# Performance work log

Measured on AMD Instinct MI355X. Metric: run time of the kernel, lower is better.

Reference implementation:

```python
import jax, jax.numpy as jnp
import numpy as np

NUM_ATOMS = 50000
NUM_EDGES = 200000  # even: edges come in (fwd, rev) pairs
D_V, D_E, D_H = 133, 14, 256
DEPTH = 3


def setup_inputs() -> dict:
    key = jax.random.key(0)
    ks = jax.random.split(key, 12)
    half = NUM_EDGES // 2
    src = jax.random.randint(ks[0], (half,), 0, NUM_ATOMS)
    dst = jax.random.randint(ks[1], (half,), 0, NUM_ATOMS)
    v = jnp.concatenate([src, dst])
    w = jnp.concatenate([dst, src])
    edge_index = jnp.stack([v, w])  # [2, E]
    rev_edge_index = jnp.concatenate([jnp.arange(half) + half, jnp.arange(half)])

    def lin(k, out_d, in_d):
        return jax.random.normal(k, (out_d, in_d), jnp.float32) / np.sqrt(in_d)

    return {
        "V": jax.random.normal(ks[2], (NUM_ATOMS, D_V), jnp.float32),
        "E_feat": jax.random.normal(ks[3], (NUM_EDGES, D_E), jnp.float32),
        "edge_index": edge_index,
        "rev_edge_index": rev_edge_index,
        "Wi_atom": lin(ks[4], D_H, D_V),
        "Wi_bond": lin(ks[5], D_H, D_V + D_E),
        "Wh_atom": lin(ks[6], D_H, D_H),
        "Wh_bond": lin(ks[7], D_H, D_H),
        "Wf_atom": lin(ks[8], D_H, D_H),
        "Wf_bond": lin(ks[9], D_H, D_H),
        "Wo_atom": lin(ks[10], D_H, D_V + D_H),
    }


def _sum_and_max_into_atoms(H_e, w_idx, num_atoms):
    a_sum = jax.ops.segment_sum(H_e, w_idx, num_segments=num_atoms)
    a_max = jax.ops.segment_max(H_e, w_idx, num_segments=num_atoms)
    a_max = jnp.where(jnp.isfinite(a_max), a_max, 0.0)  # empty segments -> 0
    return a_sum, a_max


def _fuse(H, m, Wf):
    # Fusion(kind='mlp', residual=True), dropout=0:
    # residual update with a small MLP on the combined signal
    return H + jax.nn.relu((H + m) @ Wf.T)


def reference(V, E_feat, edge_index, rev_edge_index, Wi_atom, Wi_bond,
              Wh_atom, Wh_bond, Wf_atom, Wf_bond, Wo_atom):
    tau = jax.nn.relu
    num_atoms = V.shape[0]
    v = edge_index[0]
    w = edge_index[1]

    H_a = tau(V @ Wi_atom.T)                                        # [N, d_h]
    H_b = tau(jnp.concatenate([V[v], E_feat], axis=1) @ Wi_bond.T)  # [E, d_h]

    for _ in range(1, DEPTH):
        a_sum, a_max = _sum_and_max_into_atoms(H_b, w, num_atoms)
        gate = a_sum * a_max
        m_a = gate @ Wh_atom.T
        H_a = _fuse(H_a, m_a, Wf_atom)

        M_b = a_sum[v] - H_b[rev_edge_index]
        m_b = M_b @ Wh_bond.T
        H_b = _fuse(H_b, m_b, Wf_bond)

    a_sum, _ = _sum_and_max_into_atoms(H_b, w, num_atoms)
    H_atom = tau(jnp.concatenate([V, a_sum], axis=1) @ Wo_atom.T)   # [N, d_h]
    return H_atom
```

## Files before the change

kernel.cpp:

```cpp
#include <hip/hip_runtime.h>
#include <hip/hip_bf16.h>

#define NATOM 50000
#define NEDGE 200000
#define HALF  100000
#define DV    133
#define DE    14
#define DH    256
#define KVP   160
#define NBLK_SCAN ((NATOM + 255) / 256)

typedef __bf16  bf16x8 __attribute__((ext_vector_type(8)));
typedef __bf16  bf16x4 __attribute__((ext_vector_type(4)));
typedef float   f32x4  __attribute__((ext_vector_type(4)));

__device__ __forceinline__ void gll16(const void* g, void* l) {
    __builtin_amdgcn_global_load_lds(
        (const __attribute__((address_space(1))) unsigned int*)g,
        (__attribute__((address_space(3))) unsigned int*)l, 16, 0, 0);
}
__device__ __forceinline__ void drain_barrier() {
    __builtin_amdgcn_s_waitcnt(0);
    __syncthreads();
}
__device__ __forceinline__ int swz(int row, int byteInRow) {
    return row * 512 + (byteInRow ^ ((row & 7) << 4));
}


struct DArgs {
    const float* Vf; const float* Ef; const float* asumf;
    const int* vidx;
    const __bf16* W1; const __bf16* W2;
    __bf16* C; float* Cf;
    int M;
};

template<int MODE, int KITERS>
__global__ __launch_bounds__(512, 4) void dgemm(DArgs g) {
    const int tid = threadIdx.x;
    const int lane = tid & 63, wv = tid >> 6;
    const int quad = lane >> 4, l16 = lane & 15;
    const int wr = (wv >> 2) * 64, wc = (wv & 3) * 64;
    const int gr0 = blockIdx.x * 128;

    int vrow[4]; const float* epp[4];
#pragma unroll
    for (int m = 0; m < 4; ++m) {
        int r = gr0 + wr + m * 16 + l16;
        if (r > g.M - 1) r = g.M - 1;
        vrow[m] = (MODE == 1) ? g.vidx[r] : r;
        epp[m] = (MODE == 1) ? (g.Ef + (size_t)r * DE) : nullptr;
    }

    f32x4 acc[16];
#pragma unroll
    for (int i = 0; i < 16; ++i) acc[i] = (f32x4){0.f, 0.f, 0.f, 0.f};

#pragma unroll
    for (int kk = 0; kk < KITERS; ++kk) {
        bf16x8 af[4];
#pragma unroll
        for (int m = 0; m < 4; ++m) {
            const int cb = kk * 32 + quad * 8;
            if (MODE != 2 || kk < 5) {
                const float* vp = g.Vf + (size_t)vrow[m] * DV;
                if (kk < 4) {
                    f32x4 x0, x1;
                    __builtin_memcpy(&x0, vp + cb, 16);
                    __builtin_memcpy(&x1, vp + cb + 4, 16);
#pragma unroll
                    for (int j = 0; j < 4; ++j) {
                        af[m][j] = (__bf16)x0[j]; af[m][4 + j] = (__bf16)x1[j];
                    }
                } else {
#pragma unroll
                    for (int j = 0; j < 8; ++j) {
                        int c = cb + j; float y = 0.f;
                        if (c < DV) y = vp[c];
                        else if (MODE == 1 && c < DV + DE) y = epp[m][c - DV];
                        af[m][j] = (__bf16)y;
                    }
                }
            } else {
                const float* sp = g.asumf + (size_t)vrow[m] * DH + (kk - 5) * 32 + quad * 8;
                f32x4 s0 = *(const f32x4*)sp, s1 = *(const f32x4*)(sp + 4);
#pragma unroll
                for (int j = 0; j < 4; ++j) {
                    af[m][j] = (__bf16)s0[j]; af[m][4 + j] = (__bf16)s1[j];
                }
            }
        }
        bf16x8 bfv[4];
#pragma unroll
        for (int n = 0; n < 4; ++n) {
            int col = wc + n * 16 + l16;
            const __bf16* wp;
            if (MODE == 2 && kk >= 5) wp = g.W2 + (size_t)col * DH  + (kk - 5) * 32 + quad * 8;
            else                      wp = g.W1 + (size_t)col * KVP + kk * 32 + quad * 8;
            bfv[n] = *(const bf16x8*)wp;
        }
#pragma unroll
        for (int m = 0; m < 4; ++m)
#pragma unroll
            for (int n = 0; n < 4; ++n)
                acc[m * 4 + n] = __builtin_amdgcn_mfma_f32_16x16x32_bf16(
                    af[m], bfv[n], acc[m * 4 + n], 0, 0, 0);
    }

#pragma unroll
    for (int m = 0; m < 4; ++m)
#pragma unroll
    for (int n = 0; n < 4; ++n)
#pragma unroll
    for (int r = 0; r < 4; ++r) {
        int gr = gr0 + wr + m * 16 + quad * 4 + r;
        if (gr < g.M) {
            int col = wc + n * 16 + l16;
            float v = acc[m * 4 + n][r];
            v = v > 0.f ? v : 0.f;
            if (MODE == 2) g.Cf[(size_t)gr * DH + col] = v;
            else           g.C [(size_t)gr * DH + col] = (__bf16)v;
        }
    }
}

struct FArgs {
    const float* asumf; const __bf16* asumb; const __bf16* amaxb;
    const int* vidx;
    const __bf16* W1; const __bf16* W2;
    __bf16* H;
    int M;
};

template<int BOND>
__global__ __launch_bounds__(512, 4) void fgemm(FArgs g) {
    __shared__ __bf16 Hlds[16384];
    __shared__ __bf16 Alds[16384];
    const int tid = threadIdx.x;
    const int lane = tid & 63, wv = tid >> 6;
    const int quad = lane >> 4, l16 = lane & 15;
    const int wr = (wv >> 2) * 32;
    const int wc = (wv & 3) * 64;
    const int bid = blockIdx.x;

    int garow[2];
    if (!BOND) {
#pragma unroll
        for (int fr = 0; fr < 2; ++fr) {
            int r = bid * 64 + wr + fr * 16 + l16;
            if (r > g.M - 1) r = g.M - 1;
            garow[fr] = r;
        }
    }

#pragma unroll
    for (int it = 0; it < 4; ++it) {
        int unit = it * 512 + wv * 64 + lane;
        int lr = unit >> 5, u16 = unit & 31;
        int swzoff = (u16 * 16) ^ ((lr & 7) << 4);
        int srow;
        if (BOND) { int sl = bid * 32 + (lr & 31); srow = (lr < 32) ? sl : HALF + sl; }
        else      { srow = bid * 64 + lr; if (srow > g.M - 1) srow = g.M - 1; }
        gll16((const char*)g.H + (size_t)srow * 512 + swzoff,
              (char*)Hlds + it * 8192 + wv * 1024);
        if (BOND) {
            int sl = bid * 32 + (lr & 31);
            int gA = (lr < 32) ? sl : HALF + sl;
            int grow = g.vidx[gA];
            gll16((const char*)g.asumb + (size_t)grow * 512 + swzoff,
                  (char*)Alds + it * 8192 + wv * 1024);
        }
    }
    drain_barrier();

    f32x4 acc[8];
#pragma unroll
    for (int i = 0; i < 8; ++i) acc[i] = (f32x4){0.f, 0.f, 0.f, 0.f};

#pragma unroll
    for (int kk = 0; kk < 8; ++kk) {
        const int cb = kk * 32 + quad * 8;
        bf16x8 mf[2];
#pragma unroll
        for (int fr = 0; fr < 2; ++fr) {
            int lr = wr + fr * 16 + l16;
            if (BOND) {
                bf16x8 a = *(const bf16x8*)((const char*)Alds + swz(lr, cb * 2));
                bf16x8 h = *(const bf16x8*)((const char*)Hlds + swz(lr ^ 32, cb * 2));
#pragma unroll
                for (int j = 0; j < 8; ++j)
                    mf[fr][j] = (__bf16)((float)a[j] - (float)h[j]);
            } else {
                const float* s = g.asumf + (size_t)garow[fr] * DH + cb;
                f32x4 s0 = *(const f32x4*)s, s1 = *(const f32x4*)(s + 4);
                bf16x8 mx = *(const bf16x8*)(g.amaxb + (size_t)garow[fr] * DH + cb);
#pragma unroll
                for (int j = 0; j < 4; ++j) {
                    mf[fr][j]     = (__bf16)(s0[j] * (float)mx[j]);
                    mf[fr][4 + j] = (__bf16)(s1[j] * (float)mx[4 + j]);
                }
            }
        }
        bf16x8 wf[4];
#pragma unroll
        for (int fc = 0; fc < 4; ++fc)
            wf[fc] = *(const bf16x8*)(g.W1 + (size_t)(wc + fc * 16 + l16) * DH + cb);
#pragma unroll
        for (int fc = 0; fc < 4; ++fc)
#pragma unroll
            for (int fr = 0; fr < 2; ++fr)
                acc[fc * 2 + fr] = __builtin_amdgcn_mfma_f32_16x16x32_bf16(
                    wf[fc], mf[fr], acc[fc * 2 + fr], 0, 0, 0);
    }
    drain_barrier();

#pragma unroll
    for (int fc = 0; fc < 4; ++fc)
#pragma unroll
    for (int fr = 0; fr < 2; ++fr) {
        int row = wr + fr * 16 + l16;
        int colb = wc + fc * 16 + quad * 4;
        int off = swz(row, colb * 2);
        bf16x4 h = *(const bf16x4*)((const char*)Hlds + off);
        bf16x4 t;
#pragma unroll
        for (int j = 0; j < 4; ++j)
            t[j] = (__bf16)((float)h[j] + acc[fc * 2 + fr][j]);
        *(bf16x4*)((char*)Alds + off) = t;
    }
    drain_barrier();

#pragma unroll
    for (int i = 0; i < 8; ++i) acc[i] = (f32x4){0.f, 0.f, 0.f, 0.f};
#pragma unroll
    for (int kk = 0; kk < 8; ++kk) {
        const int cb = kk * 32 + quad * 8;
        bf16x8 tf[2];
#pragma unroll
        for (int fr = 0; fr < 2; ++fr) {
            int lr = wr + fr * 16 + l16;
            tf[fr] = *(const bf16x8*)((const char*)Alds + swz(lr, cb * 2));
        }
        bf16x8 wf[4];
#pragma unroll
        for (int fc = 0; fc < 4; ++fc)
            wf[fc] = *(const bf16x8*)(g.W2 + (size_t)(wc + fc * 16 + l16) * DH + cb);
#pragma unroll
        for (int fc = 0; fc < 4; ++fc)
#pragma unroll
            for (int fr = 0; fr < 2; ++fr)
                acc[fc * 2 + fr] = __builtin_amdgcn_mfma_f32_16x16x32_bf16(
                    wf[fc], tf[fr], acc[fc * 2 + fr], 0, 0, 0);
    }

#pragma unroll
    for (int fc = 0; fc < 4; ++fc)
#pragma unroll
    for (int fr = 0; fr < 2; ++fr) {
        int row = wr + fr * 16 + l16;
        int colb = wc + fc * 16 + quad * 4;
        int off = swz(row, colb * 2);
        bf16x4 h = *(const bf16x4*)((const char*)Hlds + off);
        bf16x4 o;
#pragma unroll
        for (int j = 0; j < 4; ++j) {
            float v = acc[fc * 2 + fr][j];
            v = v > 0.f ? v : 0.f;
            o[j] = (__bf16)((float)h[j] + v);
        }
        *(bf16x4*)((char*)Hlds + off) = o;
    }
    drain_barrier();

#pragma unroll
    for (int it = 0; it < 4; ++it) {
        int unit = it * 512 + tid;
        int lr = unit >> 5, u16 = unit & 31;
        bool ok; int srow;
        if (BOND) { int sl = bid * 32 + (lr & 31); ok = true; srow = (lr < 32) ? sl : HALF + sl; }
        else      { srow = bid * 64 + lr; ok = srow < g.M; }
        if (ok) {
            bf16x8 v = *(const bf16x8*)((const char*)Hlds + swz(lr, u16 * 16));
            *(bf16x8*)((char*)g.H + (size_t)srow * 512 + u16 * 16) = v;
        }
    }
}

__global__ void count_deg(const int* __restrict__ widx, int* __restrict__ cnt) {
    int e = blockIdx.x * 256 + threadIdx.x;
    if (e < NEDGE) atomicAdd(&cnt[widx[e]], 1);
}

__global__ __launch_bounds__(256) void scan_p1(const int* __restrict__ cnt,
                                               int* __restrict__ rowptr,
                                               int* __restrict__ bsum) {
    __shared__ int sm[256];
    const int tid = threadIdx.x;
    const int i = blockIdx.x * 256 + tid;
    int v = (i < NATOM) ? cnt[i] : 0;
    sm[tid] = v;
    __syncthreads();
    for (int off = 1; off < 256; off <<= 1) {
        int t = (tid >= off) ? sm[tid - off] : 0;
        __syncthreads();
        sm[tid] += t;
        __syncthreads();
    }
    if (i < NATOM) rowptr[i] = sm[tid] - v;
    if (tid == 255) bsum[blockIdx.x] = sm[255];
}

__global__ __launch_bounds__(256) void scan_p2(int* __restrict__ bsum) {
    __shared__ int sm[256];
    const int tid = threadIdx.x;
    int v = (tid < NBLK_SCAN) ? bsum[tid] : 0;
    sm[tid] = v;
    __syncthreads();
    for (int off = 1; off < 256; off <<= 1) {
        int t = (tid >= off) ? sm[tid - off] : 0;
        __syncthreads();
        sm[tid] += t;
        __syncthreads();
    }
    if (tid < NBLK_SCAN) bsum[tid] = sm[tid] - v;
    if (tid == 255) bsum[NBLK_SCAN] = sm[255];
}

__global__ __launch_bounds__(256) void scan_p3(int* __restrict__ rowptr,
                                               int* __restrict__ cursor,
                                               const int* __restrict__ bsum) {
    const int i = blockIdx.x * 256 + threadIdx.x;
    if (i < NATOM) {
        int r = rowptr[i] + bsum[blockIdx.x];
        rowptr[i] = r;
        cursor[i] = r;
    }
    if (i == 0) rowptr[NATOM] = bsum[NBLK_SCAN];
}

__global__ void fill_csr(const int* __restrict__ widx, int* __restrict__ cursor,
                         int* __restrict__ eid) {
    int e = blockIdx.x * 256 + threadIdx.x;
    if (e >= NEDGE) return;
    int pos = atomicAdd(&cursor[widx[e]], 1);
    eid[pos] = e;
}

template<int WITHMAX>
__global__ __launch_bounds__(256) void seg_reduce(
    const __bf16* __restrict__ Hb, const int* __restrict__ rowptr,
    const int* __restrict__ eid,
    float* __restrict__ asum, __bf16* __restrict__ asumb,
    __bf16* __restrict__ amaxb)
{
    int a = blockIdx.x * 4 + (threadIdx.x >> 6);
    if (a >= NATOM) return;
    const int lane = threadIdx.x & 63;
    const int beg = rowptr[a], end = rowptr[a + 1];
    float s0 = 0.f, s1 = 0.f, s2 = 0.f, s3 = 0.f;
    float m0 = 0.f, m1 = 0.f, m2 = 0.f, m3 = 0.f;
    for (int i = beg; i < end; ++i) {
        int e = eid[i];
        bf16x4 h = *(const bf16x4*)(Hb + (size_t)e * DH + lane * 4);
        float v0 = (float)h[0], v1 = (float)h[1], v2 = (float)h[2], v3 = (float)h[3];
        s0 += v0; s1 += v1; s2 += v2; s3 += v3;
        if (WITHMAX) {
            m0 = fmaxf(m0, v0); m1 = fmaxf(m1, v1);
            m2 = fmaxf(m2, v2); m3 = fmaxf(m3, v3);
        }
    }
    size_t o = (size_t)a * DH + lane * 4;
    *(f32x4*)(asum + o) = (f32x4){s0, s1, s2, s3};
    if (WITHMAX) {
        bf16x4 sv; sv[0] = (__bf16)s0; sv[1] = (__bf16)s1; sv[2] = (__bf16)s2; sv[3] = (__bf16)s3;
        *(bf16x4*)(asumb + o) = sv;
        bf16x4 mv; mv[0] = (__bf16)m0; mv[1] = (__bf16)m1; mv[2] = (__bf16)m2; mv[3] = (__bf16)m3;
        *(bf16x4*)(amaxb + o) = mv;
    }
}

__global__ void pad_w2(const float* __restrict__ src, __bf16* __restrict__ dst,
                       int srcld, int coloff, int KS, int KD) {
    int i = blockIdx.x * 256 + threadIdx.x;
    if (i >= 256 * KD) return;
    int n = i / KD, c = i - n * KD;
    dst[i] = (c < KS) ? (__bf16)src[(size_t)n * srcld + coloff + c] : (__bf16)0.f;
}

static inline int cdiv(long a, long b) { return (int)((a + b - 1) / b); }

extern "C" void kernel_launch(void* const* d_in, const int* in_sizes, int n_in,
                              void* d_out, int out_size, void* d_ws, size_t ws_size,
                              hipStream_t stream) {
    const float* V    = (const float*)d_in[0];
    const float* Ef   = (const float*)d_in[1];
    const int*   ei   = (const int*)d_in[2];
    const int*   rev  = (const int*)d_in[3];
    const float* Wi_a = (const float*)d_in[4];
    const float* Wi_b = (const float*)d_in[5];
    const float* Wh_a = (const float*)d_in[6];
    const float* Wh_b = (const float*)d_in[7];
    const float* Wf_a = (const float*)d_in[8];
    const float* Wf_b = (const float*)d_in[9];
    const float* Wo   = (const float*)d_in[10];
    float* out = (float*)d_out;
    (void)rev;

    const int* vidx = ei;
    const int* widx = ei + NEDGE;

    char* ws = (char*)d_ws;
    __bf16* Hb    = (__bf16*)(ws + 0);
    __bf16* Ha    = (__bf16*)(ws + 102400000);
    float*  asum  = (float*) (ws + 128000000);
    __bf16* asumb = (__bf16*)(ws + 179200000);
    __bf16* amaxb = (__bf16*)(ws + 204800000);
    __bf16* Wia   = (__bf16*)(ws + 230400000);
    __bf16* Wib   = (__bf16*)(ws + 230481920);
    __bf16* Wo1   = (__bf16*)(ws + 230563840);
    __bf16* Wo2   = (__bf16*)(ws + 230645760);
    __bf16* Wha   = (__bf16*)(ws + 230776832);
    __bf16* Whb   = (__bf16*)(ws + 230907904);
    __bf16* Wfa   = (__bf16*)(ws + 231038976);
    __bf16* Wfb   = (__bf16*)(ws + 231170048);
    int*  rowptr  = (int*)(ws + 231301120);
    int*  cursor  = (int*)(ws + 231501312);
    int*  eid     = (int*)(ws + 231701504);
    int*  bsum    = (int*)(ws + 232501504);
    (void)ws_size;

    hipMemsetAsync(cursor, 0, NATOM * sizeof(int), stream);
    count_deg<<<cdiv(NEDGE, 256), 256, 0, stream>>>(widx, cursor);
    scan_p1<<<NBLK_SCAN, 256, 0, stream>>>(cursor, rowptr, bsum);
    scan_p2<<<1, 256, 0, stream>>>(bsum);
    scan_p3<<<NBLK_SCAN, 256, 0, stream>>>(rowptr, cursor, bsum);
    fill_csr<<<cdiv(NEDGE, 256), 256, 0, stream>>>(widx, cursor, eid);

    pad_w2<<<cdiv(256 * KVP, 256), 256, 0, stream>>>(Wi_a, Wia, DV, 0, DV, KVP);
    pad_w2<<<cdiv(256 * KVP, 256), 256, 0, stream>>>(Wi_b, Wib, DV + DE, 0, DV + DE, KVP);
    pad_w2<<<cdiv(256 * KVP, 256), 256, 0, stream>>>(Wo, Wo1, DV + DH, 0, DV, KVP);
    pad_w2<<<cdiv(256 * DH, 256), 256, 0, stream>>>(Wo, Wo2, DV + DH, DV, DH, DH);
    pad_w2<<<cdiv(256 * DH, 256), 256, 0, stream>>>(Wh_a, Wha, DH, 0, DH, DH);
    pad_w2<<<cdiv(256 * DH, 256), 256, 0, stream>>>(Wh_b, Whb, DH, 0, DH, DH);
    pad_w2<<<cdiv(256 * DH, 256), 256, 0, stream>>>(Wf_a, Wfa, DH, 0, DH, DH);
    pad_w2<<<cdiv(256 * DH, 256), 256, 0, stream>>>(Wf_b, Wfb, DH, 0, DH, DH);

    {
        DArgs d{}; d.Vf = V; d.W1 = Wia; d.C = Ha; d.M = NATOM;
        dgemm<0, 5><<<cdiv(NATOM, 128), 512, 0, stream>>>(d);
    }
    {
        DArgs d{}; d.Vf = V; d.Ef = Ef; d.vidx = vidx; d.W1 = Wib; d.C = Hb; d.M = NEDGE;
        dgemm<1, 5><<<cdiv(NEDGE, 128), 512, 0, stream>>>(d);
    }

    for (int it = 0; it < 2; ++it) {
        seg_reduce<1><<<cdiv(NATOM, 4), 256, 0, stream>>>(Hb, rowptr, eid, asum, asumb, amaxb);
        {
            FArgs f{}; f.asumf = asum; f.amaxb = amaxb;
            f.W1 = Wha; f.W2 = Wfa; f.H = Ha; f.M = NATOM;
            fgemm<0><<<cdiv(NATOM, 64), 512, 0, stream>>>(f);
        }
        {
            FArgs f{}; f.asumb = asumb; f.vidx = vidx;
            f.W1 = Whb; f.W2 = Wfb; f.H = Hb; f.M = HALF;
            fgemm<1><<<HALF / 32, 512, 0, stream>>>(f);
        }
    }

    seg_reduce<0><<<cdiv(NATOM, 4), 256, 0, stream>>>(Hb, rowptr, eid, asum, nullptr, nullptr);
    {
        DArgs d{}; d.Vf = V; d.asumf = asum; d.W1 = Wo1; d.W2 = Wo2; d.Cf = out; d.M = NATOM;
        dgemm<2, 13><<<cdiv(NATOM, 128), 512, 0, stream>>>(d);
    }
}
```

Measured before the change: 1.134 ms.

## Merge atom and bond fusion GEMMs into one launch with smaller tiles

Merges the separate atom and bond fused-MLP GEMM kernels into one launch that picks the branch by block index. It also halves the row tile per block (64 to 32 atom rows, 32 to 16 bond pairs), which halves LDS use and raises the occupancy hint to 8 blocks. The goal is to cut a launch per iteration, let the two independent workloads overlap, and improve latency hiding through more resident blocks. The cost is that each weight fragment loaded from global memory now feeds half as many MFMAs, so weight traffic per output row doubles.

New measurement: 1.482 ms. 1.31x slower.

```diff
diff --git a/kernel.cpp b/kernel.cpp
--- a/kernel.cpp
+++ b/kernel.cpp
@@ -125,48 +125,48 @@
     }
 }
 
-struct FArgs {
+struct F2Args {
     const float* asumf; const __bf16* asumb; const __bf16* amaxb;
     const int* vidx;
-    const __bf16* W1; const __bf16* W2;
-    __bf16* H;
-    int M;
+    const __bf16* W1a; const __bf16* W2a;
+    const __bf16* W1b; const __bf16* W2b;
+    __bf16* Ha; __bf16* Hb;
+    int nA;
 };
 
 template<int BOND>
-__global__ __launch_bounds__(512, 4) void fgemm(FArgs g) {
-    __shared__ __bf16 Hlds[16384];
-    __shared__ __bf16 Alds[16384];
+__device__ __forceinline__ void fgemm_body(const F2Args& g, int bid,
+                                           __bf16* Hlds, __bf16* Alds) {
     const int tid = threadIdx.x;
     const int lane = tid & 63, wv = tid >> 6;
     const int quad = lane >> 4, l16 = lane & 15;
-    const int wr = (wv >> 2) * 32;
+    const int wr = (wv >> 2) * 16;
     const int wc = (wv & 3) * 64;
-    const int bid = blockIdx.x;
-
-    int garow[2];
+    __bf16* H        = BOND ? g.Hb  : g.Ha;
+    const __bf16* W1 = BOND ? g.W1b : g.W1a;
+    const __bf16* W2 = BOND ? g.W2b : g.W2a;
+    const int M      = BOND ? HALF  : NATOM;
+
+    int garow = 0;
     if (!BOND) {
-#pragma unroll
-        for (int fr = 0; fr < 2; ++fr) {
-            int r = bid * 64 + wr + fr * 16 + l16;
-            if (r > g.M - 1) r = g.M - 1;
-            garow[fr] = r;
-        }
-    }
-
-#pragma unroll
-    for (int it = 0; it < 4; ++it) {
+        int r = bid * 32 + wr + l16;
+        if (r > M - 1) r = M - 1;
+        garow = r;
+    }
+
+#pragma unroll
+    for (int it = 0; it < 2; ++it) {
         int unit = it * 512 + wv * 64 + lane;
         int lr = unit >> 5, u16 = unit & 31;
         int swzoff = (u16 * 16) ^ ((lr & 7) << 4);
         int srow;
-        if (BOND) { int sl = bid * 32 + (lr & 31); srow = (lr < 32) ? sl : HALF + sl; }
-        else      { srow = bid * 64 + lr; if (srow > g.M - 1) srow = g.M - 1; }
-        gll16((const char*)g.H + (size_t)srow * 512 + swzoff,
+        if (BOND) { int sl = bid * 16 + (lr & 15); srow = (lr < 16) ? sl : HALF + sl; }
+        else      { srow = bid * 32 + lr; if (srow > M - 1) srow = M - 1; }
+        gll16((const char*)H + (size_t)srow * 512 + swzoff,
               (char*)Hlds + it * 8192 + wv * 1024);
         if (BOND) {
-            int sl = bid * 32 + (lr & 31);
-            int gA = (lr < 32) ? sl : HALF + sl;
+            int sl = bid * 16 + (lr & 15);
+            int gA = (lr < 16) ? sl : HALF + sl;
             int grow = g.vidx[gA];
             gll16((const char*)g.asumb + (size_t)grow * 512 + swzoff,
                   (char*)Alds + it * 8192 + wv * 1024);
@@ -174,98 +174,84 @@
     }
     drain_barrier();
 
-    f32x4 acc[8];
-#pragma unroll
-    for (int i = 0; i < 8; ++i) acc[i] = (f32x4){0.f, 0.f, 0.f, 0.f};
+    f32x4 acc[4];
+#pragma unroll
+    for (int i = 0; i < 4; ++i) acc[i] = (f32x4){0.f, 0.f, 0.f, 0.f};
 
 #pragma unroll
     for (int kk = 0; kk < 8; ++kk) {
         const int cb = kk * 32 + quad * 8;
-        bf16x8 mf[2];
-#pragma unroll
-        for (int fr = 0; fr < 2; ++fr) {
-            int lr = wr + fr * 16 + l16;
+        bf16x8 mf;
+        {
+            int lr = wr + l16;
             if (BOND) {
                 bf16x8 a = *(const bf16x8*)((const char*)Alds + swz(lr, cb * 2));
-                bf16x8 h = *(const bf16x8*)((const char*)Hlds + swz(lr ^ 32, cb * 2));
+                bf16x8 h = *(const bf16x8*)((const char*)Hlds + swz(lr ^ 16, cb * 2));
 #pragma unroll
                 for (int j = 0; j < 8; ++j)
-                    mf[fr][j] = (__bf16)((float)a[j] - (float)h[j]);
+                    mf[j] = (__bf16)((float)a[j] - (float)h[j]);
             } else {
-                const float* s = g.asumf + (size_t)garow[fr] * DH + cb;
+                const float* s = g.asumf + (size_t)garow * DH + cb;
                 f32x4 s0 = *(const f32x4*)s, s1 = *(const f32x4*)(s + 4);
-                bf16x8 mx = *(const bf16x8*)(g.amaxb + (size_t)garow[fr] * DH + cb);
+                bf16x8 mx = *(const bf16x8*)(g.amaxb + (size_t)garow * DH + cb);
 #pragma unroll
                 for (int j = 0; j < 4; ++j) {
-                    mf[fr][j]     = (__bf16)(s0[j] * (float)mx[j]);
-                    mf[fr][4 + j] = (__bf16)(s1[j] * (float)mx[4 + j]);
+                    mf[j]     = (__bf16)(s0[j] * (float)mx[j]);
+                    mf[4 + j] = (__bf16)(s1[j] * (float)mx[4 + j]);
                 }
             }
         }
         bf16x8 wf[4];
 #pragma unroll
         for (int fc = 0; fc < 4; ++fc)
-            wf[fc] = *(const bf16x8*)(g.W1 + (size_t)(wc + fc * 16 + l16) * DH + cb);
+            wf[fc] = *(const bf16x8*)(W1 + (size_t)(wc + fc * 16 + l16) * DH + cb);
 #pragma unroll
         for (int fc = 0; fc < 4; ++fc)
-#pragma unroll
-            for (int fr = 0; fr < 2; ++fr)
-                acc[fc * 2 + fr] = __builtin_amdgcn_mfma_f32_16x16x32_bf16(
-                    wf[fc], mf[fr], acc[fc * 2 + fr], 0, 0, 0);
+            acc[fc] = __builtin_amdgcn_mfma_f32_16x16x32_bf16(
+                wf[fc], mf, acc[fc], 0, 0, 0);
     }
     drain_barrier();
 
 #pragma unroll
-    for (int fc = 0; fc < 4; ++fc)
-#pragma unroll
-    for (int fr = 0; fr < 2; ++fr) {
-        int row = wr + fr * 16 + l16;
+    for (int fc = 0; fc < 4; ++fc) {
+        int row = wr + l16;
         int colb = wc + fc * 16 + quad * 4;
         int off = swz(row, colb * 2);
         bf16x4 h = *(const bf16x4*)((const char*)Hlds + off);
         bf16x4 t;
 #pragma unroll
         for (int j = 0; j < 4; ++j)
-            t[j] = (__bf16)((float)h[j] + acc[fc * 2 + fr][j]);
+            t[j] = (__bf16)((float)h[j] + acc[fc][j]);
         *(bf16x4*)((char*)Alds + off) = t;
     }
     drain_barrier();
 
 #pragma unroll
-    for (int i = 0; i < 8; ++i) acc[i] = (f32x4){0.f, 0.f, 0.f, 0.f};
+    for (int i = 0; i < 4; ++i) acc[i] = (f32x4){0.f, 0.f, 0.f, 0.f};
 #pragma unroll
     for (int kk = 0; kk < 8; ++kk) {
         const int cb = kk * 32 + quad * 8;
-        bf16x8 tf[2];
-#pragma unroll
-        for (int fr = 0; fr < 2; ++fr) {
-            int lr = wr + fr * 16 + l16;
-            tf[fr] = *(const bf16x8*)((const char*)Alds + swz(lr, cb * 2));
-        }
+        bf16x8 tf = *(const bf16x8*)((const char*)Alds + swz(wr + l16, cb * 2));
         bf16x8 wf[4];
 #pragma unroll
         for (int fc = 0; fc < 4; ++fc)
-            wf[fc] = *(const bf16x8*)(g.W2 + (size_t)(wc + fc * 16 + l16) * DH + cb);
+            wf[fc] = *(const bf16x8*)(W2 + (size_t)(wc + fc * 16 + l16) * DH + cb);
 #pragma unroll
         for (int fc = 0; fc < 4; ++fc)
-#pragma unroll
-            for (int fr = 0; fr < 2; ++fr)
-                acc[fc * 2 + fr] = __builtin_amdgcn_mfma_f32_16x16x32_bf16(
-                    wf[fc], tf[fr], acc[fc * 2 + fr], 0, 0, 0);
-    }
-
-#pragma unroll
-    for (int fc = 0; fc < 4; ++fc)
-#pragma unroll
-    for (int fr = 0; fr < 2; ++fr) {
-        int row = wr + fr * 16 + l16;
+            acc[fc] = __builtin_amdgcn_mfma_f32_16x16x32_bf16(
+                wf[fc], tf, acc[fc], 0, 0, 0);
+    }
+
+#pragma unroll
+    for (int fc = 0; fc < 4; ++fc) {
+        int row = wr + l16;
         int colb = wc + fc * 16 + quad * 4;
         int off = swz(row, colb * 2);
         bf16x4 h = *(const bf16x4*)((const char*)Hlds + off);
         bf16x4 o;
 #pragma unroll
         for (int j = 0; j < 4; ++j) {
-            float v = acc[fc * 2 + fr][j];
+            float v = acc[fc][j];
             v = v > 0.f ? v : 0.f;
             o[j] = (__bf16)((float)h[j] + v);
         }
@@ -274,17 +260,25 @@
     drain_barrier();
 
 #pragma unroll
-    for (int it = 0; it < 4; ++it) {
+    for (int it = 0; it < 2; ++it) {
         int unit = it * 512 + tid;
         int lr = unit >> 5, u16 = unit & 31;
         bool ok; int srow;
-        if (BOND) { int sl = bid * 32 + (lr & 31); ok = true; srow = (lr < 32) ? sl : HALF + sl; }
-        else      { srow = bid * 64 + lr; ok = srow < g.M; }
+        if (BOND) { int sl = bid * 16 + (lr & 15); ok = true; srow = (lr < 16) ? sl : HALF + sl; }
+        else      { srow = bid * 32 + lr; ok = srow < M; }
         if (ok) {
             bf16x8 v = *(const bf16x8*)((const char*)Hlds + swz(lr, u16 * 16));
-            *(bf16x8*)((char*)g.H + (size_t)srow * 512 + u16 * 16) = v;
-        }
-    }
+            *(bf16x8*)((char*)H + (size_t)srow * 512 + u16 * 16) = v;
+        }
+    }
+}
+
+__global__ __launch_bounds__(512, 8) void fgemm2(F2Args g) {
+    __shared__ __bf16 Hlds[8192];
+    __shared__ __bf16 Alds[8192];
+    const int bid = blockIdx.x;
+    if (bid < g.nA) fgemm_body<0>(g, bid, Hlds, Alds);
+    else            fgemm_body<1>(g, bid - g.nA, Hlds, Alds);
 }
 
 __global__ void count_deg(const int* __restrict__ widx, int* __restrict__ cnt) {
@@ -455,18 +449,15 @@
         dgemm<1, 5><<<cdiv(NEDGE, 128), 512, 0, stream>>>(d);
     }
 
+    const int nA = cdiv(NATOM, 32);
+    const int nB = HALF / 16;
     for (int it = 0; it < 2; ++it) {
         seg_reduce<1><<<cdiv(NATOM, 4), 256, 0, stream>>>(Hb, rowptr, eid, asum, asumb, amaxb);
-        {
-            FArgs f{}; f.asumf = asum; f.amaxb = amaxb;
-            f.W1 = Wha; f.W2 = Wfa; f.H = Ha; f.M = NATOM;
-            fgemm<0><<<cdiv(NATOM, 64), 512, 0, stream>>>(f);
-        }
-        {
-            FArgs f{}; f.asumb = asumb; f.vidx = vidx;
-            f.W1 = Whb; f.W2 = Wfb; f.H = Hb; f.M = HALF;
-            fgemm<1><<<HALF / 32, 512, 0, stream>>>(f);
-        }
+        F2Args f{};
+        f.asumf = asum; f.asumb = asumb; f.amaxb = amaxb; f.vidx = vidx;
+        f.W1a = Wha; f.W2a = Wfa; f.W1b = Whb; f.W2b = Wfb;
+        f.Ha = Ha; f.Hb = Hb; f.nA = nA;
+        fgemm2<<<nA + nB, 512, 0, stream>>>(f);
     }
 
     seg_reduce<0><<<cdiv(NATOM, 4), 256, 0, stream>>>(Hb, rowptr, eid, asum, nullptr, nullptr);
```
